# Kernel tuning notes

Measured on AMD Instinct MI355X. Metric: run time of the kernel, lower is better.

## Reference

```python
import jax, jax.numpy as jnp
import numpy as np

RADIUS = 64
STRIDE = RADIUS // 2
EPS = 1e-5

def box_filter(x, w):
    # depthwise conv: groups=3, RADIUSxRADIUS kernel of ones, stride RADIUS//2, no padding
    return jax.lax.conv_general_dilated(
        x, w, window_strides=(STRIDE, STRIDE), padding='VALID',
        feature_group_count=3, dimension_numbers=('NCHW', 'OIHW', 'NCHW'))

def conv1x1(x, w):
    # 1x1 conv == per-pixel matmul over channels
    return jnp.einsum('bchw,oc->bohw', x, w)

def batchnorm(x, g, b):
    # BatchNorm2d in training mode: biased batch stats over (N,H,W)
    m = jnp.mean(x, axis=(0, 2, 3), keepdims=True)
    v = jnp.var(x, axis=(0, 2, 3), keepdims=True)
    return (x - m) * jax.lax.rsqrt(v + EPS) * g[None, :, None, None] + b[None, :, None, None]

def resize_bilinear_ac(x, oh, ow):
    # F.interpolate(mode='bilinear', align_corners=True), separable gathers
    B, C, h, w = x.shape
    ys = jnp.linspace(0.0, h - 1.0, oh)
    y0 = jnp.floor(ys).astype(jnp.int32)
    y1 = jnp.minimum(y0 + 1, h - 1)
    wy = (ys - y0.astype(x.dtype))[None, None, :, None]
    xh = jnp.take(x, y0, axis=2) * (1 - wy) + jnp.take(x, y1, axis=2) * wy
    xs = jnp.linspace(0.0, w - 1.0, ow)
    x0 = jnp.floor(xs).astype(jnp.int32)
    x1 = jnp.minimum(x0 + 1, w - 1)
    wx = (xs - x0.astype(x.dtype))[None, None, None, :]
    return jnp.take(xh, x0, axis=3) * (1 - wx) + jnp.take(xh, x1, axis=3) * wx

def setup_inputs():
    key = jax.random.key(0)
    ks = jax.random.split(key, 5)
    B, H, W = 4, 1024, 1024
    guide = jax.random.uniform(ks[0], (B, 3, H, W), dtype=jnp.float32)
    src = jax.random.uniform(ks[1], (B, 3, H, W), dtype=jnp.float32)
    box_w = jnp.ones((3, 1, RADIUS, RADIUS), jnp.float32)  # weight.data[...] = 1.0
    w1 = jax.random.normal(ks[2], (32, 6), jnp.float32) * 0.2
    w2 = jax.random.normal(ks[3], (32, 32), jnp.float32) * 0.2
    w3 = jax.random.normal(ks[4], (3, 32), jnp.float32) * 0.2
    g1 = jnp.ones((32,), jnp.float32); b1 = jnp.zeros((32,), jnp.float32)
    g2 = jnp.ones((32,), jnp.float32); b2 = jnp.zeros((32,), jnp.float32)
    return dict(guide=guide, src=src, box_w=box_w, w1=w1, g1=g1, b1=b1,
                w2=w2, g2=g2, b2=b2, w3=w3)

def reference(guide, src, box_w, w1, g1, b1, w2, g2, b2, w3):
    B, C, H, W = guide.shape
    N = box_filter(jnp.ones((1, 3, H, W), guide.dtype), box_w)  # local window counts
    mean_x = box_filter(guide, box_w) / N
    mean_y = box_filter(src, box_w) / N
    cov_xy = box_filter(guide * src, box_w) / N - mean_x * mean_y
    var_x = box_filter(guide * guide, box_w) / N - mean_x * mean_x
    h = jnp.concatenate([cov_xy, var_x], axis=1)  # [B,6,h',w']
    h = jax.nn.relu(batchnorm(conv1x1(h, w1), g1, b1))
    h = jax.nn.relu(batchnorm(conv1x1(h, w2), g2, b2))
    A = conv1x1(h, w3)  # [B,3,h',w']
    b = mean_y - A * mean_x
    mean_A = resize_bilinear_ac(A, H, W)
    mean_b = resize_bilinear_ac(b, H, W)
    return mean_A * guide + mean_b
```

## Files before the change

### kernel.cpp

```cpp
#include <hip/hip_runtime.h>
#include <stdint.h>

#define B_      4
#define C_      3
#define H_      1024
#define W_      1024
#define OH_     31
#define NHS_    64
#define NP_     3844
#define NPOSPB_ 961
#define EPS_    1e-5f

#define NBLK_MID 16

#define TILE_PLANE 24576
#define OFF_TILE  0
#define OFF_STATS 98304
#define OFF_BAR   98432
#define OFF_A     98436
#define OFF_BV    109968

typedef float f4 __attribute__((ext_vector_type(4)));

__global__ __launch_bounds__(256) void k1_tilesums(
        const float* __restrict__ g,
        const float* __restrict__ s,
        float* __restrict__ ws) {
    int blk = blockIdx.x;
    int bc = blk >> 6;
    int hs = blk & 63;
    int t  = threadIdx.x;
    const f4* gp = (const f4*)(g + ((size_t)bc * H_ + (size_t)hs * 16) * W_);
    const f4* sp = (const f4*)(s + ((size_t)bc * H_ + (size_t)hs * 16) * W_);
    float sg = 0.f, ss = 0.f, sgs = 0.f, sgg = 0.f;
#pragma unroll 4
    for (int r = 0; r < 16; r++) {
        f4 gv = gp[r * (W_ / 4) + t];
        f4 sv = __builtin_nontemporal_load(sp + r * (W_ / 4) + t);
        sg  += (gv.x + gv.y) + (gv.z + gv.w);
        ss  += (sv.x + sv.y) + (sv.z + sv.w);
        sgs += gv.x * sv.x + gv.y * sv.y + gv.z * sv.z + gv.w * sv.w;
        sgg += gv.x * gv.x + gv.y * gv.y + gv.z * gv.z + gv.w * gv.w;
    }
#pragma unroll
    for (int off = 4; off; off >>= 1) {
        sg  += __shfl_down(sg,  off, 8);
        ss  += __shfl_down(ss,  off, 8);
        sgs += __shfl_down(sgs, off, 8);
        sgg += __shfl_down(sgg, off, 8);
    }
    if ((t & 7) == 0) {
        int tx = t >> 3;
        int base = (bc * NHS_ + hs) * 32 + tx;
        ws[OFF_TILE + 0 * TILE_PLANE + base] = sg;
        ws[OFF_TILE + 1 * TILE_PLANE + base] = ss;
        ws[OFF_TILE + 2 * TILE_PLANE + base] = sgs;
        ws[OFF_TILE + 3 * TILE_PLANE + base] = sgg;
    }
    if (blk == 0 && t < 132) ws[OFF_STATS + t] = 0.f;
}

__device__ __forceinline__ void bar16(float* ws, int idx) {
    __syncthreads();
    if (threadIdx.x == 0) {
        __threadfence();
        int* ctr = (int*)(ws + OFF_BAR) + idx;
        __atomic_fetch_add(ctr, 1, __ATOMIC_ACQ_REL);
        while (__hip_atomic_load(ctr, __ATOMIC_ACQUIRE, __HIP_MEMORY_SCOPE_AGENT) < NBLK_MID) {
            __builtin_amdgcn_s_sleep(2);
        }
    }
    __syncthreads();
}

__global__ __launch_bounds__(256) void kmid(
        const float* __restrict__ w1f,
        const float* __restrict__ g1f,
        const float* __restrict__ b1f,
        const float* __restrict__ w2f,
        const float* __restrict__ g2f,
        const float* __restrict__ b2f,
        const float* __restrict__ w3f,
        float* __restrict__ ws) {
    __shared__ float red[4][64];
    __shared__ float scs[32], shs[32];
    int t  = threadIdx.x;
    int wv = t >> 6, ln = t & 63;
    int p  = blockIdx.x * 256 + t;
    bool ok = p < NP_;
    int pp = ok ? p : 0;
    int b  = pp / NPOSPB_;
    int r  = pp % NPOSPB_;
    int oy = r / OH_, ox = r % OH_;

    float h[6], mxv[3], myv[3];
#pragma unroll
    for (int c = 0; c < 3; c++) {
        int bc = b * 3 + c;
        int base = (bc * NHS_ + oy * 2) * 32 + ox;
        float S[4];
#pragma unroll
        for (int pl = 0; pl < 4; pl++) {
            const float* tp = ws + OFF_TILE + pl * TILE_PLANE + base;
            S[pl] = ((tp[0]  + tp[1])  + (tp[32] + tp[33]))
                  + ((tp[64] + tp[65]) + (tp[96] + tp[97]));
        }
        const float inv = 1.f / 4096.f;
        float mx = S[0] * inv, my = S[1] * inv;
        h[c]     = S[2] * inv - mx * my;
        h[3 + c] = S[3] * inv - mx * mx;
        mxv[c] = mx; myv[c] = my;
    }
    float a[32];
#pragma unroll
    for (int o = 0; o < 32; o++) {
        float y = 0.f;
#pragma unroll
        for (int i = 0; i < 6; i++) y += w1f[o * 6 + i] * h[i];
        a[o] = y;
    }

#pragma unroll
    for (int o = 0; o < 32; o++) {
        float sv = ok ? a[o] : 0.f;
        float sq = sv * sv;
#pragma unroll
        for (int off = 32; off; off >>= 1) {
            sv += __shfl_down(sv, off, 64);
            sq += __shfl_down(sq, off, 64);
        }
        if (ln == 0) { red[wv][o] = sv; red[wv][32 + o] = sq; }
    }
    __syncthreads();
    if (t < 64) {
        float tot = red[0][t] + red[1][t] + red[2][t] + red[3][t];
        atomicAdd(&ws[OFF_STATS + t], tot);
    }
    bar16(ws, 0);

    if (t < 32) {
        float sm = __hip_atomic_load(&ws[OFF_STATS + t],      __ATOMIC_RELAXED, __HIP_MEMORY_SCOPE_AGENT);
        float sq = __hip_atomic_load(&ws[OFF_STATS + 32 + t], __ATOMIC_RELAXED, __HIP_MEMORY_SCOPE_AGENT);
        float m = sm * (1.f / NP_);
        float v = sq * (1.f / NP_) - m * m;
        float sc = g1f[t] * rsqrtf(v + EPS_);
        scs[t] = sc; shs[t] = b1f[t] - m * sc;
    }
    __syncthreads();

#pragma unroll
    for (int i = 0; i < 32; i++) a[i] = fmaxf(a[i] * scs[i] + shs[i], 0.f);
    float y2[32];
#pragma unroll
    for (int o = 0; o < 32; o++) {
        float y = 0.f;
#pragma unroll
        for (int i = 0; i < 32; i++) y += w2f[o * 32 + i] * a[i];
        y2[o] = y;
    }

#pragma unroll
    for (int o = 0; o < 32; o++) {
        float sv = ok ? y2[o] : 0.f;
        float sq = sv * sv;
#pragma unroll
        for (int off = 32; off; off >>= 1) {
            sv += __shfl_down(sv, off, 64);
            sq += __shfl_down(sq, off, 64);
        }
        if (ln == 0) { red[wv][o] = sv; red[wv][32 + o] = sq; }
    }
    __syncthreads();
    if (t < 64) {
        float tot = red[0][t] + red[1][t] + red[2][t] + red[3][t];
        atomicAdd(&ws[OFF_STATS + 64 + t], tot);
    }
    bar16(ws, 1);

    if (t < 32) {
        float sm = __hip_atomic_load(&ws[OFF_STATS + 64 + t], __ATOMIC_RELAXED, __HIP_MEMORY_SCOPE_AGENT);
        float sq = __hip_atomic_load(&ws[OFF_STATS + 96 + t], __ATOMIC_RELAXED, __HIP_MEMORY_SCOPE_AGENT);
        float m = sm * (1.f / NP_);
        float v = sq * (1.f / NP_) - m * m;
        float sc = g2f[t] * rsqrtf(v + EPS_);
        scs[t] = sc; shs[t] = b2f[t] - m * sc;
    }
    __syncthreads();

#pragma unroll
    for (int i = 0; i < 32; i++) y2[i] = fmaxf(y2[i] * scs[i] + shs[i], 0.f);
    if (ok) {
#pragma unroll
        for (int c = 0; c < 3; c++) {
            float av = 0.f;
#pragma unroll
            for (int i = 0; i < 32; i++) av += w3f[c * 32 + i] * y2[i];
            ws[OFF_A  + c * NP_ + p] = av;
            ws[OFF_BV + c * NP_ + p] = myv[c] - av * mxv[c];
        }
    }
}

__global__ __launch_bounds__(256) void k5_final(
        const float* __restrict__ g,
        const float* __restrict__ ws,
        float* __restrict__ out) {
    int blk = blockIdx.x;
    int y  = blk & 1023;
    int bc = blk >> 10;
    int b = bc / 3, c = bc % 3;
    float fy = (float)y * (30.f / 1023.f);
    int y0 = (int)fy;
    float wy = fy - (float)y0;
    int y1i = min(y0 + 1, 30);
    const float* A0 = ws + OFF_A  + c * NP_ + b * NPOSPB_ + y0  * OH_;
    const float* A1 = ws + OFF_A  + c * NP_ + b * NPOSPB_ + y1i * OH_;
    const float* B0 = ws + OFF_BV + c * NP_ + b * NPOSPB_ + y0  * OH_;
    const float* B1 = ws + OFF_BV + c * NP_ + b * NPOSPB_ + y1i * OH_;
    int t = threadIdx.x;
    size_t rowoff = ((size_t)bc * H_ + (size_t)y) * W_;
    const f4* gp = (const f4*)(g + rowoff);
    f4* op = (f4*)(out + rowoff);
    f4 gv = gp[t];
    float go[4] = { gv.x, gv.y, gv.z, gv.w };
    float r[4];
#pragma unroll
    for (int j = 0; j < 4; j++) {
        int x = t * 4 + j;
        float fx = (float)x * (30.f / 1023.f);
        int x0 = (int)fx;
        float wx = fx - (float)x0;
        int x1 = min(x0 + 1, 30);
        float a  = (A0[x0] * (1.f - wx) + A0[x1] * wx) * (1.f - wy)
                 + (A1[x0] * (1.f - wx) + A1[x1] * wx) * wy;
        float bb = (B0[x0] * (1.f - wx) + B0[x1] * wx) * (1.f - wy)
                 + (B1[x0] * (1.f - wx) + B1[x1] * wx) * wy;
        r[j] = a * go[j] + bb;
    }
    f4 ov;
    ov.x = r[0]; ov.y = r[1]; ov.z = r[2]; ov.w = r[3];
    __builtin_nontemporal_store(ov, op + t);
}

extern "C" void kernel_launch(void* const* d_in, const int* in_sizes, int n_in,
                              void* d_out, int out_size, void* d_ws, size_t ws_size,
                              hipStream_t stream) {
    const float* guide = (const float*)d_in[0];
    const float* src   = (const float*)d_in[1];
    const float* w1 = (const float*)d_in[3];
    const float* g1 = (const float*)d_in[4];
    const float* b1 = (const float*)d_in[5];
    const float* w2 = (const float*)d_in[6];
    const float* g2 = (const float*)d_in[7];
    const float* b2 = (const float*)d_in[8];
    const float* w3 = (const float*)d_in[9];
    float* ws = (float*)d_ws;
    float* out = (float*)d_out;

    hipLaunchKernelGGL(k1_tilesums, dim3(B_ * C_ * NHS_), dim3(256), 0, stream, guide, src, ws);
    hipLaunchKernelGGL(kmid,        dim3(NBLK_MID),       dim3(256), 0, stream,
                       w1, g1, b1, w2, g2, b2, w3, ws);
    hipLaunchKernelGGL(k5_final,    dim3(B_ * C_ * H_),   dim3(256), 0, stream, guide, ws, out);
}
```

Baseline: 200.0 us.

## Split mid-stage channel work across four waves per position via LDS exchange

The MLP/batchnorm kernel grows from 256 to 1024 threads per block. Each group of four waves shares the same 256 positions, and each wave computes 8 of the 32 output channels. The ReLU activations are exchanged through a padded shared-memory buffer so every thread can read the full 32-wide input for the next 1x1 conv. This cuts per-thread serial FMA and shuffle-reduction work in the latency-bound 16-block stage, at the cost of extra LDS traffic and barriers. The grid-barrier spin sleep is also shortened.

Result: faster. 181.8 us (-9.1%).

```diff
diff --git a/kernel.cpp b/kernel.cpp
--- a/kernel.cpp
+++ b/kernel.cpp
@@ -67,13 +67,13 @@
         int* ctr = (int*)(ws + OFF_BAR) + idx;
         __atomic_fetch_add(ctr, 1, __ATOMIC_ACQ_REL);
         while (__hip_atomic_load(ctr, __ATOMIC_ACQUIRE, __HIP_MEMORY_SCOPE_AGENT) < NBLK_MID) {
-            __builtin_amdgcn_s_sleep(2);
-        }
-    }
-    __syncthreads();
-}
-
-__global__ __launch_bounds__(256) void kmid(
+            __builtin_amdgcn_s_sleep(1);
+        }
+    }
+    __syncthreads();
+}
+
+__global__ __launch_bounds__(1024) void kmid(
         const float* __restrict__ w1f,
         const float* __restrict__ g1f,
         const float* __restrict__ b1f,
@@ -82,16 +82,21 @@
         const float* __restrict__ b2f,
         const float* __restrict__ w3f,
         float* __restrict__ ws) {
-    __shared__ float red[4][64];
+    __shared__ float zbuf[256 * 33];
+    __shared__ float red[16][16];
     __shared__ float scs[32], shs[32];
-    int t  = threadIdx.x;
-    int wv = t >> 6, ln = t & 63;
-    int p  = blockIdx.x * 256 + t;
-    bool ok = p < NP_;
-    int pp = ok ? p : 0;
-    int b  = pp / NPOSPB_;
-    int r  = pp % NPOSPB_;
-    int oy = r / OH_, ox = r % OH_;
+    int t    = threadIdx.x;
+    int w    = t >> 6;
+    int lane = t & 63;
+    int k    = w & 3;
+    int ko8  = __builtin_amdgcn_readfirstlane(k * 8);
+    int pl   = (w >> 2) * 64 + lane;
+    int p    = blockIdx.x * 256 + pl;
+    bool ok  = p < NP_;
+    int pp   = ok ? p : 0;
+    int b    = pp / NPOSPB_;
+    int r    = pp % NPOSPB_;
+    int oy   = r / OH_, ox = r % OH_;
 
     float h[6], mxv[3], myv[3];
 #pragma unroll
@@ -100,10 +105,10 @@
         int base = (bc * NHS_ + oy * 2) * 32 + ox;
         float S[4];
 #pragma unroll
-        for (int pl = 0; pl < 4; pl++) {
-            const float* tp = ws + OFF_TILE + pl * TILE_PLANE + base;
-            S[pl] = ((tp[0]  + tp[1])  + (tp[32] + tp[33]))
-                  + ((tp[64] + tp[65]) + (tp[96] + tp[97]));
+        for (int plane = 0; plane < 4; plane++) {
+            const float* tp = ws + OFF_TILE + plane * TILE_PLANE + base;
+            S[plane] = ((tp[0]  + tp[1])  + (tp[32] + tp[33]))
+                     + ((tp[64] + tp[65]) + (tp[96] + tp[97]));
         }
         const float inv = 1.f / 4096.f;
         float mx = S[0] * inv, my = S[1] * inv;
@@ -111,30 +116,37 @@
         h[3 + c] = S[3] * inv - mx * mx;
         mxv[c] = mx; myv[c] = my;
     }
-    float a[32];
-#pragma unroll
-    for (int o = 0; o < 32; o++) {
+    float a[8];
+#pragma unroll
+    for (int j = 0; j < 8; j++) {
         float y = 0.f;
 #pragma unroll
-        for (int i = 0; i < 6; i++) y += w1f[o * 6 + i] * h[i];
-        a[o] = y;
-    }
-
-#pragma unroll
-    for (int o = 0; o < 32; o++) {
-        float sv = ok ? a[o] : 0.f;
-        float sq = sv * sv;
+        for (int i = 0; i < 6; i++) y += w1f[(ko8 + j) * 6 + i] * h[i];
+        a[j] = y;
+    }
+
+    {
+        float sv[8], sq[8];
+#pragma unroll
+        for (int j = 0; j < 8; j++) { sv[j] = ok ? a[j] : 0.f; sq[j] = sv[j] * sv[j]; }
 #pragma unroll
         for (int off = 32; off; off >>= 1) {
-            sv += __shfl_down(sv, off, 64);
-            sq += __shfl_down(sq, off, 64);
-        }
-        if (ln == 0) { red[wv][o] = sv; red[wv][32 + o] = sq; }
+#pragma unroll
+            for (int j = 0; j < 8; j++) {
+                sv[j] += __shfl_down(sv[j], off, 64);
+                sq[j] += __shfl_down(sq[j], off, 64);
+            }
+        }
+        if (lane == 0) {
+#pragma unroll
+            for (int j = 0; j < 8; j++) { red[w][j] = sv[j]; red[w][8 + j] = sq[j]; }
+        }
     }
     __syncthreads();
     if (t < 64) {
-        float tot = red[0][t] + red[1][t] + red[2][t] + red[3][t];
-        atomicAdd(&ws[OFF_STATS + t], tot);
+        int o = t & 31; int kk = o >> 3; int col = ((t >= 32) ? 8 : 0) + (o & 7);
+        float tot = red[kk][col] + red[kk + 4][col] + red[kk + 8][col] + red[kk + 12][col];
+        atomicAdd(&ws[OFF_STATS + ((t >= 32) ? 32 : 0) + o], tot);
     }
     bar16(ws, 0);
 
@@ -149,31 +161,45 @@
     __syncthreads();
 
 #pragma unroll
-    for (int i = 0; i < 32; i++) a[i] = fmaxf(a[i] * scs[i] + shs[i], 0.f);
-    float y2[32];
-#pragma unroll
-    for (int o = 0; o < 32; o++) {
+    for (int j = 0; j < 8; j++) {
+        float zz = fmaxf(a[j] * scs[ko8 + j] + shs[ko8 + j], 0.f);
+        zbuf[pl * 33 + ko8 + j] = zz;
+    }
+    __syncthreads();
+    float zal[32];
+#pragma unroll
+    for (int i = 0; i < 32; i++) zal[i] = zbuf[pl * 33 + i];
+    float y2[8];
+#pragma unroll
+    for (int j = 0; j < 8; j++) {
         float y = 0.f;
 #pragma unroll
-        for (int i = 0; i < 32; i++) y += w2f[o * 32 + i] * a[i];
-        y2[o] = y;
-    }
-
-#pragma unroll
-    for (int o = 0; o < 32; o++) {
-        float sv = ok ? y2[o] : 0.f;
-        float sq = sv * sv;
+        for (int i = 0; i < 32; i++) y += w2f[(ko8 + j) * 32 + i] * zal[i];
+        y2[j] = y;
+    }
+
+    {
+        float sv[8], sq[8];
+#pragma unroll
+        for (int j = 0; j < 8; j++) { sv[j] = ok ? y2[j] : 0.f; sq[j] = sv[j] * sv[j]; }
 #pragma unroll
         for (int off = 32; off; off >>= 1) {
-            sv += __shfl_down(sv, off, 64);
-            sq += __shfl_down(sq, off, 64);
-        }
-        if (ln == 0) { red[wv][o] = sv; red[wv][32 + o] = sq; }
+#pragma unroll
+            for (int j = 0; j < 8; j++) {
+                sv[j] += __shfl_down(sv[j], off, 64);
+                sq[j] += __shfl_down(sq[j], off, 64);
+            }
+        }
+        if (lane == 0) {
+#pragma unroll
+            for (int j = 0; j < 8; j++) { red[w][j] = sv[j]; red[w][8 + j] = sq[j]; }
+        }
     }
     __syncthreads();
     if (t < 64) {
-        float tot = red[0][t] + red[1][t] + red[2][t] + red[3][t];
-        atomicAdd(&ws[OFF_STATS + 64 + t], tot);
+        int o = t & 31; int kk = o >> 3; int col = ((t >= 32) ? 8 : 0) + (o & 7);
+        float tot = red[kk][col] + red[kk + 4][col] + red[kk + 8][col] + red[kk + 12][col];
+        atomicAdd(&ws[OFF_STATS + 64 + ((t >= 32) ? 32 : 0) + o], tot);
     }
     bar16(ws, 1);
 
@@ -188,13 +214,20 @@
     __syncthreads();
 
 #pragma unroll
-    for (int i = 0; i < 32; i++) y2[i] = fmaxf(y2[i] * scs[i] + shs[i], 0.f);
-    if (ok) {
+    for (int j = 0; j < 8; j++) {
+        float zz = fmaxf(y2[j] * scs[ko8 + j] + shs[ko8 + j], 0.f);
+        zbuf[pl * 33 + ko8 + j] = zz;
+    }
+    __syncthreads();
+    if (k == 0 && ok) {
+        float z2[32];
+#pragma unroll
+        for (int i = 0; i < 32; i++) z2[i] = zbuf[pl * 33 + i];
 #pragma unroll
         for (int c = 0; c < 3; c++) {
             float av = 0.f;
 #pragma unroll
-            for (int i = 0; i < 32; i++) av += w3f[c * 32 + i] * y2[i];
+            for (int i = 0; i < 32; i++) av += w3f[c * 32 + i] * z2[i];
             ws[OFF_A  + c * NP_ + p] = av;
             ws[OFF_BV + c * NP_ + p] = myv[c] - av * mxv[c];
         }
@@ -257,8 +290,8 @@
     float* ws = (float*)d_ws;
     float* out = (float*)d_out;
 
-    hipLaunchKernelGGL(k1_tilesums, dim3(B_ * C_ * NHS_), dim3(256), 0, stream, guide, src, ws);
-    hipLaunchKernelGGL(kmid,        dim3(NBLK_MID),       dim3(256), 0, stream,
+    hipLaunchKernelGGL(k1_tilesums, dim3(B_ * C_ * NHS_), dim3(256),  0, stream, guide, src, ws);
+    hipLaunchKernelGGL(kmid,        dim3(NBLK_MID),       dim3(1024), 0, stream,
                        w1, g1, b1, w2, g2, b2, w3, ws);
-    hipLaunchKernelGGL(k5_final,    dim3(B_ * C_ * H_),   dim3(256), 0, stream, guide, ws, out);
-}
+    hipLaunchKernelGGL(k5_final,    dim3(B_ * C_ * H_),   dim3(256),  0, stream, guide, ws, out);
+}
```
